# Kernel tuning notes

Hardware: AMD Instinct MI355X
Metric: run time of the kernel (lower is better)

The kernel has to match this reference:

```python
import jax, jax.numpy as jnp
import numpy as np
import math

B = 2
D_MODEL = 2048
L_MAX = 4096
FILTER_ORDER = 64
EMB_DIM = 3
SHORT_K = 3


def setup_inputs() -> dict:
    key = jax.random.key(0)
    ks = jax.random.split(key, 16)
    D = D_MODEL

    def n(k, shape, scale=0.02):
        return jax.random.normal(k, shape, dtype=jnp.float32) * scale

    return {
        "x": jax.random.normal(ks[0], (B, L_MAX, D), dtype=jnp.float32),
        "in_proj_w": n(ks[1], (3 * D, D)),
        "in_proj_b": n(ks[2], (3 * D,)),
        "short_w": n(ks[3], (3 * D, 1, SHORT_K), 0.3),   # depthwise conv weight (O, I/groups=1, K)
        "short_b": n(ks[4], (3 * D,), 0.1),
        "mlp_w0": n(ks[5], (FILTER_ORDER, EMB_DIM), 0.5),
        "mlp_b0": n(ks[6], (FILTER_ORDER,), 0.5),
        "sin_freq": jnp.ones((1, FILTER_ORDER), dtype=jnp.float32),  # Sin module, w=1, shared across MLP layers
        "mlp_w1": n(ks[7], (FILTER_ORDER, FILTER_ORDER), 0.1),
        "mlp_b1": n(ks[8], (FILTER_ORDER,), 0.1),
        "mlp_w2": n(ks[9], (FILTER_ORDER, FILTER_ORDER), 0.1),
        "mlp_b2": n(ks[10], (FILTER_ORDER,), 0.1),
        "mlp_w3": n(ks[11], (D, FILTER_ORDER), 0.1),      # final Linear(order -> d_model, bias=False)
        "filter_bias": jax.random.normal(ks[12], (D,), dtype=jnp.float32),  # HyenaFilter.bias ~ randn
        "out_proj_w": n(ks[13], (D, D)),
        "out_proj_b": n(ks[14], (D,)),
    }


def _pos_emb(L):
    # PositionalEmbedding: t in [0,1], 1 complex band (emb_dim=3 -> bands=1)
    t = jnp.linspace(0.0, 1.0, L)[:, None]               # (L, 1)
    t_resc = jnp.linspace(0.0, L - 1.0, L)
    w = 2.0 * math.pi * t_resc / L                       # (L,)
    bands = (EMB_DIM - 1) // 2
    f = jnp.linspace(1e-4, bands - 1.0, bands)           # (bands,)
    ang = f[None, :] * w[:, None]                        # (L, bands)
    # z = exp(-1j * f * w) -> real = cos, imag = -sin
    z = jnp.concatenate([t, jnp.cos(ang), -jnp.sin(ang)], axis=-1)  # (L, 3)
    return z, t


def _filter_k(L, w0, b0, freq, w1, b1, w2, b2, w3):
    z, t = _pos_emb(L)
    h = jnp.sin(freq * (z @ w0.T + b0))
    h = jnp.sin(freq * (h @ w1.T + b1))
    h = jnp.sin(freq * (h @ w2.T + b2))
    h = h @ w3.T                                         # (L, D)
    # ExponentialModulation: deltas = linspace(log(.01)/1.5, log(.01)/0.3, D)
    max_decay = math.log(0.01) / 0.3
    min_decay = math.log(0.01) / 1.5
    deltas = jnp.linspace(min_decay, max_decay, h.shape[-1])
    decay = jnp.exp(-t * jnp.abs(deltas)[None, :])       # (L, D)
    return (h * decay).T                                 # (D, L)


def _fftconv(u, k, bias):
    # fftconv_ref with gelu=False, no dropout_mask: u (B, D, L), k (D, L), bias (D,)
    L = u.shape[-1]
    n = 2 * L
    k_f = jnp.fft.rfft(k, n=n) / n                       # (D, L+1)
    u_f = jnp.fft.rfft(u, n=n)                           # (B, D, L+1)
    y = jnp.fft.irfft(u_f * k_f, n=n, norm="forward")[..., :L]
    return y + u * bias[:, None]


def reference(x, in_proj_w, in_proj_b, short_w, short_b, mlp_w0, mlp_b0, sin_freq,
              mlp_w1, mlp_b1, mlp_w2, mlp_b2, mlp_w3, filter_bias,
              out_proj_w, out_proj_b):
    Bn, L, D = x.shape
    u = x @ in_proj_w.T + in_proj_b                      # (B, L, 3D)
    u = jnp.transpose(u, (0, 2, 1))                      # (B, 3D, L)
    # depthwise short conv, padding = short_k - 1, truncate to L (causal-ish)
    uc = jax.lax.conv_general_dilated(
        u, short_w, window_strides=(1,),
        padding=[(SHORT_K - 1, SHORT_K - 1)],
        feature_group_count=3 * D,
        dimension_numbers=("NCH", "OIH", "NCH"))
    uc = uc[..., :L] + short_b[None, :, None]
    x0, x1, v = jnp.split(uc, 3, axis=1)                 # each (B, D, L)
    k = _filter_k(L, mlp_w0, mlp_b0, sin_freq, mlp_w1, mlp_b1, mlp_w2, mlp_b2, mlp_w3)
    # order=2 Hyena recurrence: single gated long-conv step
    v = v * x1
    v = _fftconv(v, k, filter_bias)
    y = v * x0                                           # (B, D, L)
    y = jnp.transpose(y, (0, 2, 1))                      # (B, L, D)
    return y @ out_proj_w.T + out_proj_b
```

## Files before the change

### kernel.cpp

```cpp
#include <hip/hip_runtime.h>
#include <hip/hip_bf16.h>
#include <cstdint>
#include <cstddef>

typedef __attribute__((ext_vector_type(8))) short    bf16x8;
typedef __attribute__((ext_vector_type(4))) float    f32x4;
typedef __attribute__((ext_vector_type(8))) unsigned short u16x8;
typedef __attribute__((ext_vector_type(4))) float    f32v4;
typedef __attribute__((ext_vector_type(4))) unsigned short u16v4;

__device__ __forceinline__ float b2f(unsigned short v) {
    return __builtin_bit_cast(float, ((unsigned int)v) << 16);
}
__device__ __forceinline__ unsigned short f2b(float f) {
    unsigned int u = __builtin_bit_cast(unsigned int, f);
    u += 0x7fffu + ((u >> 16) & 1u);
    return (unsigned short)(u >> 16);
}

__device__ __forceinline__ void async16(const void* g, void* l) {
    __builtin_amdgcn_global_load_lds(
        (const __attribute__((address_space(1))) unsigned int*)g,
        (__attribute__((address_space(3))) unsigned int*)l, 16, 0, 0);
}

__global__ __launch_bounds__(256) void cvt_f32_bf16(const float* __restrict__ src,
                                                    unsigned short* __restrict__ dst, int n4) {
    int i = blockIdx.x * blockDim.x + threadIdx.x;
    int stride = gridDim.x * blockDim.x;
    const f32v4* s4 = (const f32v4*)src;
    u16v4* d4 = (u16v4*)dst;
    for (; i < n4; i += stride) {
        f32v4 v = s4[i];
        u16v4 o;
        o.x = f2b(v.x); o.y = f2b(v.y); o.z = f2b(v.z); o.w = f2b(v.w);
        d4[i] = o;
    }
}

template <int MODE>
__global__ __launch_bounds__(256, 2) void gemm_bf16(
    const unsigned short* __restrict__ A,
    const unsigned short* __restrict__ Bw,
    const float* __restrict__ bias,
    void* __restrict__ Cout,
    int M, int N, int K, int Lseq, int CH)
{
    constexpr int SMEM_N = (MODE == 1) ? 16384 : 8192;
    __shared__ unsigned short smem[SMEM_N];

    const int tid  = threadIdx.x;
    const int w    = tid >> 6;
    const int lane = tid & 63;
    const int quad = lane >> 4;
    const int lq   = lane & 15;
    const int n0 = blockIdx.x * 128;
    const int m0 = blockIdx.y * 128;
    const int wave_m = w & 1, wave_n = w >> 1;

    const int rSub = w * 32 + (lane >> 2);
    const int kcol = (lane & 3) * 8;
    const unsigned short* pA0 = A  + (size_t)(m0 + rSub)      * K + kcol;
    const unsigned short* pA1 = A  + (size_t)(m0 + rSub + 16) * K + kcol;
    const unsigned short* pB0 = Bw + (size_t)(n0 + rSub)      * K + kcol;
    const unsigned short* pB1 = Bw + (size_t)(n0 + rSub + 16) * K + kcol;
    char* sb = (char*)smem;
    char* dA0 = sb + w * 2048;
    char* dA1 = sb + w * 2048 + 1024;
    char* dB0 = sb + 8192 + w * 2048;
    char* dB1 = sb + 8192 + w * 2048 + 1024;

    f32x4 acc[4][4] = {};

    const int nIter = K >> 5;
    for (int kt = 0; kt < nIter; ++kt) {
        async16(pA0, dA0); async16(pA1, dA1);
        async16(pB0, dB0); async16(pB1, dB1);
        pA0 += 32; pA1 += 32; pB0 += 32; pB1 += 32;
        __syncthreads();
        bf16x8 af[4], bw[4];
        #pragma unroll
        for (int i = 0; i < 4; ++i) {
            af[i] = *(const bf16x8*)&smem[(wave_m * 64 + i * 16 + lq) * 32 + quad * 8];
            bw[i] = *(const bf16x8*)&smem[4096 + (wave_n * 64 + i * 16 + lq) * 32 + quad * 8];
        }
        #pragma unroll
        for (int i = 0; i < 4; ++i)
            #pragma unroll
            for (int j = 0; j < 4; ++j)
                acc[i][j] = __builtin_amdgcn_mfma_f32_16x16x32_bf16(af[i], bw[j], acc[i][j], 0, 0, 0);
        __syncthreads();
    }

    if (MODE == 0) {
        float* out = (float*)Cout;
        #pragma unroll
        for (int j = 0; j < 4; ++j) {
            const int col = n0 + wave_n * 64 + j * 16 + lq;
            const float bv = bias[col];
            #pragma unroll
            for (int i = 0; i < 4; ++i) {
                const int rowb = m0 + wave_m * 64 + i * 16 + quad * 4;
                f32x4 c = acc[i][j];
                out[(size_t)(rowb + 0) * N + col] = c.x + bv;
                out[(size_t)(rowb + 1) * N + col] = c.y + bv;
                out[(size_t)(rowb + 2) * N + col] = c.z + bv;
                out[(size_t)(rowb + 3) * N + col] = c.w + bv;
            }
        }
    } else {
        #pragma unroll
        for (int j = 0; j < 4; ++j) {
            const int nl = wave_n * 64 + j * 16 + lq;
            const float bv = bias[n0 + nl];
            #pragma unroll
            for (int i = 0; i < 4; ++i) {
                const int ml = wave_m * 64 + i * 16 + quad * 4;
                f32x4 c = acc[i][j];
                smem[nl * 128 + ml + 0] = f2b(c.x + bv);
                smem[nl * 128 + ml + 1] = f2b(c.y + bv);
                smem[nl * 128 + ml + 2] = f2b(c.z + bv);
                smem[nl * 128 + ml + 3] = f2b(c.w + bv);
            }
        }
        __syncthreads();
        unsigned short* uo = (unsigned short*)Cout;
        const int bI = m0 >> 12;
        const int l0 = m0 & 4095;
        for (int e = tid; e < 2048; e += 256) {
            const int nl = e >> 4, seg = e & 15;
            u16x8 v = *(const u16x8*)&smem[nl * 128 + seg * 8];
            *(u16x8*)&uo[(size_t)(bI * CH + n0 + nl) * Lseq + l0 + seg * 8] = v;
        }
    }
}

__global__ __launch_bounds__(256) void filter_kernel(
    const float* __restrict__ w0, const float* __restrict__ b0,
    const float* __restrict__ freq,
    const float* __restrict__ w1, const float* __restrict__ b1,
    const float* __restrict__ w2, const float* __restrict__ b2,
    const float* __restrict__ w3, float* __restrict__ kf)
{
    __shared__ float ha[64][64];
    __shared__ float hb[64][64];
    const int tid = threadIdx.x;
    const int l0 = blockIdx.x * 64;
    const int d0 = blockIdx.y * 256;
    const int l  = tid & 63;
    const int lg = l0 + l;
    const float tt = (float)lg * (1.0f / 4095.0f);
    const float wang = 6.283185307179586f * (float)lg * (1.0f / 4096.0f);
    const float a  = 1e-4f * wang;
    const float z0 = tt, z1 = cosf(a), z2 = -sinf(a);

    for (int e = tid; e < 4096; e += 256) {
        const int dim = e >> 6;
        float pre = z0 * w0[dim * 3] + z1 * w0[dim * 3 + 1] + z2 * w0[dim * 3 + 2] + b0[dim];
        ha[dim][l] = sinf(freq[dim] * pre);
    }
    __syncthreads();
    for (int e = tid; e < 4096; e += 256) {
        const int dim = e >> 6;
        float acc = b1[dim];
        #pragma unroll
        for (int jj = 0; jj < 64; ++jj) acc += w1[dim * 64 + jj] * ha[jj][l];
        hb[dim][l] = sinf(freq[dim] * acc);
    }
    __syncthreads();
    for (int e = tid; e < 4096; e += 256) {
        const int dim = e >> 6;
        float acc = b2[dim];
        #pragma unroll
        for (int jj = 0; jj < 64; ++jj) acc += w2[dim * 64 + jj] * hb[jj][l];
        ha[dim][l] = sinf(freq[dim] * acc);
    }
    __syncthreads();
    for (int d = d0 + (tid >> 6); d < d0 + 256; d += 4) {
        float acc = 0.f;
        #pragma unroll
        for (int jj = 0; jj < 64; ++jj) acc += w3[d * 64 + jj] * ha[jj][l];
        const float delta = fabsf(-3.0701134573253944f + (-5.999245642062483e-3f) * (float)d);
        kf[(size_t)d * 4096 + lg] = acc * __expf(-tt * delta);
    }
}

#define PIDX(i) ((i) + ((i) >> 5))

__device__ __forceinline__ void bfly_f(float& r1, float& i1, float& r2, float& i2, float wr, float wi) {
    float ur = r1, ui = i1, vr = r2, vi = i2;
    r1 = ur + vr; i1 = ui + vi;
    float dr = ur - vr, di = ui - vi;
    r2 = dr * wr - di * wi;
    i2 = dr * wi + di * wr;
}
__device__ __forceinline__ void bfly_i(float& r1, float& i1, float& r2, float& i2, float wr, float wi) {
    float vr = r2 * wr - i2 * wi, vi = r2 * wi + i2 * wr;
    float ur = r1, ui = i1;
    r1 = ur + vr; i1 = ui + vi;
    r2 = ur - vr; i2 = ui - vi;
}

template <int DS, int STR>
__device__ __forceinline__ void fwd_stage(float* re, float* im, int tt) {
    float wr[8], wi[8];
    constexpr float c = -3.14159265358979f / (float)(STR * DS);
    #pragma unroll
    for (int k = 0; k < DS; ++k) __sincosf(c * (float)(tt + STR * k), &wi[k], &wr[k]);
    #pragma unroll
    for (int s = 0; s < 16; ++s)
        if ((s & DS) == 0)
            bfly_f(re[s], im[s], re[s + DS], im[s + DS], wr[s & (DS - 1)], wi[s & (DS - 1)]);
}
template <int DS, int STR>
__device__ __forceinline__ void inv_stage(float* re, float* im, int tt) {
    float wr[8], wi[8];
    constexpr float c = 3.14159265358979f / (float)(STR * DS);
    #pragma unroll
    for (int k = 0; k < DS; ++k) __sincosf(c * (float)(tt + STR * k), &wi[k], &wr[k]);
    #pragma unroll
    for (int s = 0; s < 16; ++s)
        if ((s & DS) == 0)
            bfly_i(re[s], im[s], re[s + DS], im[s + DS], wr[s & (DS - 1)], wi[s & (DS - 1)]);
}

__device__ __forceinline__ void xchg(float* re, float* im, float* fre, float* fim,
                                     int wbase, int wstr, int rbase, int rstr) {
    __syncthreads();
    #pragma unroll
    for (int s = 0; s < 16; ++s) {
        const int i = wbase + wstr * s;
        fre[PIDX(i)] = re[s]; fim[PIDX(i)] = im[s];
    }
    __syncthreads();
    #pragma unroll
    for (int s = 0; s < 16; ++s) {
        const int i = rbase + rstr * s;
        re[s] = fre[PIDX(i)]; im[s] = fim[PIDX(i)];
    }
}

__device__ __forceinline__ void fwd_fft(float* re, float* im, float* fre, float* fim, int t) {
    const int off = t & 31, seg = t >> 5;
    fwd_stage<8, 512>(re, im, t);
    fwd_stage<4, 512>(re, im, t);
    fwd_stage<2, 512>(re, im, t);
    fwd_stage<1, 512>(re, im, t);
    xchg(re, im, fre, fim, t, 512, seg * 512 + off, 32);
    fwd_stage<8, 32>(re, im, off);
    fwd_stage<4, 32>(re, im, off);
    fwd_stage<2, 32>(re, im, off);
    fwd_stage<1, 32>(re, im, off);
    {
        float wr, wi;
        __sincosf(-3.14159265358979f * (float)(off & 15) / 16.0f, &wi, &wr);
        const bool hi = (off & 16) != 0;
        #pragma unroll
        for (int s = 0; s < 16; ++s) {
            float rr = __shfl_xor(re[s], 16);
            float ri = __shfl_xor(im[s], 16);
            if (!hi) { re[s] += rr; im[s] += ri; }
            else {
                float dr = rr - re[s], di = ri - im[s];
                re[s] = dr * wr - di * wi;
                im[s] = dr * wi + di * wr;
            }
        }
    }
    xchg(re, im, fre, fim, seg * 512 + off, 32, 16 * t, 1);
    fwd_stage<8, 1>(re, im, 0);
    fwd_stage<4, 1>(re, im, 0);
    fwd_stage<2, 1>(re, im, 0);
    fwd_stage<1, 1>(re, im, 0);
}

__device__ __forceinline__ void inv_fft(float* re, float* im, float* fre, float* fim, int t) {
    const int off = t & 31, seg = t >> 5;
    inv_stage<1, 1>(re, im, 0);
    inv_stage<2, 1>(re, im, 0);
    inv_stage<4, 1>(re, im, 0);
    inv_stage<8, 1>(re, im, 0);
    xchg(re, im, fre, fim, 16 * t, 1, seg * 512 + off, 32);
    {
        float wr, wi;
        __sincosf(3.14159265358979f * (float)(off & 15) / 16.0f, &wi, &wr);
        const bool hi = (off & 16) != 0;
        #pragma unroll
        for (int s = 0; s < 16; ++s) {
            float rr = __shfl_xor(re[s], 16);
            float ri = __shfl_xor(im[s], 16);
            if (!hi) {
                float vr = rr * wr - ri * wi, vi = rr * wi + ri * wr;
                re[s] += vr; im[s] += vi;
            } else {
                float vr = re[s] * wr - im[s] * wi, vi = re[s] * wi + im[s] * wr;
                re[s] = rr - vr; im[s] = ri - vi;
            }
        }
    }
    inv_stage<1, 32>(re, im, off);
    inv_stage<2, 32>(re, im, off);
    inv_stage<4, 32>(re, im, off);
    inv_stage<8, 32>(re, im, off);
    xchg(re, im, fre, fim, seg * 512 + off, 32, t, 512);
    inv_stage<1, 512>(re, im, t);
    inv_stage<2, 512>(re, im, t);
    inv_stage<4, 512>(re, im, t);
    inv_stage<8, 512>(re, im, t);
}

__global__ __launch_bounds__(512, 2) void kfft_kernel(
    const float* __restrict__ kf,
    float* __restrict__ kspec)
{
    __shared__ float fre[8448];
    __shared__ float fim[8448];
    const int t = threadIdx.x;
    const int d = blockIdx.x;
    float kr[16], ki[16];
    #pragma unroll
    for (int s = 0; s < 16; ++s) {
        kr[s] = (s < 8) ? kf[(size_t)d * 4096 + t + 512 * s] : 0.f;
        ki[s] = 0.f;
    }
    fwd_fft(kr, ki, fre, fim, t);
    f32x4* kv = (f32x4*)kspec + (size_t)d * 4096 + t;
    #pragma unroll
    for (int q = 0; q < 8; ++q) {
        f32x4 o;
        o.x = kr[2 * q]; o.y = ki[2 * q];
        o.z = kr[2 * q + 1]; o.w = ki[2 * q + 1];
        kv[q * 512] = o;
    }
}

__global__ __launch_bounds__(512, 2) void hyena_fft_kernel(
    const unsigned short* __restrict__ u,
    const float* __restrict__ kspec,
    const float* __restrict__ sw,
    const float* __restrict__ sbv,
    const float* __restrict__ fbias,
    unsigned short* __restrict__ zb)
{
    __shared__ float fre[8448];
    __shared__ float fim[8448];
    const int t = threadIdx.x;
    const int d = blockIdx.x;

    const int c0 = d, c1 = 2048 + d, c2 = 4096 + d;
    const float w00 = sw[c0*3+0], w01 = sw[c0*3+1], w02 = sw[c0*3+2], bb0 = sbv[c0];
    const float w10 = sw[c1*3+0], w11 = sw[c1*3+1], w12 = sw[c1*3+2], bb1 = sbv[c1];
    const float w20 = sw[c2*3+0], w21 = sw[c2*3+1], w22 = sw[c2*3+2], bb2 = sbv[c2];
    const float fb = fbias[d];

    float vgr_[2][8], x0r_[2][8];
    float xr[16], xi[16];
    #pragma unroll
    for (int s = 0; s < 8; ++s) {
        const int l = t + (s << 9);
        #pragma unroll
        for (int b = 0; b < 2; ++b) {
            const size_t base = (size_t)b * 6144 * 4096;
            const size_t r0 = base + (size_t)c0 * 4096;
            const size_t r1 = base + (size_t)c1 * 4096;
            const size_t r2 = base + (size_t)c2 * 4096;
            const float a0 = b2f(u[r0 + l]);
            const float a1 = (l >= 1) ? b2f(u[r0 + l - 1]) : 0.f;
            const float a2 = (l >= 2) ? b2f(u[r0 + l - 2]) : 0.f;
            const float x0v = w00 * a2 + w01 * a1 + w02 * a0 + bb0;
            const float e0 = b2f(u[r1 + l]);
            const float e1 = (l >= 1) ? b2f(u[r1 + l - 1]) : 0.f;
            const float e2 = (l >= 2) ? b2f(u[r1 + l - 2]) : 0.f;
            const float x1v = w10 * e2 + w11 * e1 + w12 * e0 + bb1;
            const float g0 = b2f(u[r2 + l]);
            const float g1 = (l >= 1) ? b2f(u[r2 + l - 1]) : 0.f;
            const float g2 = (l >= 2) ? b2f(u[r2 + l - 2]) : 0.f;
            const float vv = w20 * g2 + w21 * g1 + w22 * g0 + bb2;
            const float vg = vv * x1v;
            vgr_[b][s] = vg; x0r_[b][s] = x0v;
            if (b == 0) xr[s] = vg; else xi[s] = vg;
        }
    }
    #pragma unroll
    for (int s = 8; s < 16; ++s) { xr[s] = 0.f; xi[s] = 0.f; }

    fwd_fft(xr, xi, fre, fim, t);
    {
        const f32x4* kv = (const f32x4*)kspec + (size_t)d * 4096 + t;
        f32x4 kk[8];
        #pragma unroll
        for (int q = 0; q < 8; ++q) kk[q] = kv[q * 512];
        #pragma unroll
        for (int q = 0; q < 8; ++q) {
            float cr = xr[2 * q], ci = xi[2 * q];
            xr[2 * q] = cr * kk[q].x - ci * kk[q].y;
            xi[2 * q] = cr * kk[q].y + ci * kk[q].x;
            cr = xr[2 * q + 1]; ci = xi[2 * q + 1];
            xr[2 * q + 1] = cr * kk[q].z - ci * kk[q].w;
            xi[2 * q + 1] = cr * kk[q].w + ci * kk[q].z;
        }
    }
    inv_fft(xr, xi, fre, fim, t);

    const float inv_n = 1.0f / 8192.0f;
    #pragma unroll
    for (int s = 0; s < 8; ++s) {
        const int p = t + (s << 9);
        const float z0 = (xr[s] * inv_n + vgr_[0][s] * fb) * x0r_[0][s];
        const float z1 = (xi[s] * inv_n + vgr_[1][s] * fb) * x0r_[1][s];
        zb[(size_t)d * 4096 + p]          = f2b(z0);
        zb[(size_t)(2048 + d) * 4096 + p] = f2b(z1);
    }
}

__global__ __launch_bounds__(256) void transpose_kernel(const unsigned short* __restrict__ zb,
                                                        unsigned short* __restrict__ zt)
{
    __shared__ unsigned int tile[64][65];
    const int l0 = blockIdx.x * 64, d0 = blockIdx.y * 64, b = blockIdx.z;
    const int tid = threadIdx.x;
    for (int e = tid; e < 4096; e += 256) {
        const int r = e >> 6, c = e & 63;
        tile[r][c] = zb[(size_t)(b * 2048 + d0 + r) * 4096 + l0 + c];
    }
    __syncthreads();
    for (int e = tid; e < 4096; e += 256) {
        const int r = e >> 6, c = e & 63;
        zt[(size_t)(b * 4096 + l0 + r) * 2048 + d0 + c] = (unsigned short)tile[c][r];
    }
}

extern "C" void kernel_launch(void* const* d_in, const int* in_sizes, int n_in,
                              void* d_out, int out_size, void* d_ws, size_t ws_size,
                              hipStream_t stream)
{
    const float* x   = (const float*)d_in[0];
    const float* ipw = (const float*)d_in[1];
    const float* ipb = (const float*)d_in[2];
    const float* sw  = (const float*)d_in[3];
    const float* sb  = (const float*)d_in[4];
    const float* w0  = (const float*)d_in[5];
    const float* b0  = (const float*)d_in[6];
    const float* fr  = (const float*)d_in[7];
    const float* w1  = (const float*)d_in[8];
    const float* b1  = (const float*)d_in[9];
    const float* w2  = (const float*)d_in[10];
    const float* b2  = (const float*)d_in[11];
    const float* w3  = (const float*)d_in[12];
    const float* fb  = (const float*)d_in[13];
    const float* opw = (const float*)d_in[14];
    const float* opb = (const float*)d_in[15];
    float* out = (float*)d_out;

    char* ws = (char*)d_ws;
    unsigned short* xb    = (unsigned short*)ws;
    unsigned short* wbi   = (unsigned short*)(ws + 33554432);
    float*          kspec = (float*)ws;
    unsigned short* ztb   = (unsigned short*)ws;
    unsigned short* wbo   = (unsigned short*)(ws + 33554432);
    unsigned short* ub    = (unsigned short*)(ws + 134217728);
    float*          kf    = (float*)(ws + 234881024);
    unsigned short* zbm   = (unsigned short*)(ws + 234881024);

    cvt_f32_bf16<<<1024, 256, 0, stream>>>(x,   xb,  16777216 / 4);
    cvt_f32_bf16<<<1024, 256, 0, stream>>>(ipw, wbi, 12582912 / 4);

    gemm_bf16<1><<<dim3(48, 64), 256, 0, stream>>>(xb, wbi, ipb, ub, 8192, 6144, 2048, 4096, 6144);

    filter_kernel<<<dim3(64, 8), 256, 0, stream>>>(w0, b0, fr, w1, b1, w2, b2, w3, kf);

    kfft_kernel<<<2048, 512, 0, stream>>>(kf, kspec);

    hyena_fft_kernel<<<2048, 512, 0, stream>>>(ub, kspec, sw, sb, fb, zbm);

    transpose_kernel<<<dim3(64, 32, 2), 256, 0, stream>>>(zbm, ztb);

    cvt_f32_bf16<<<512,  256, 0, stream>>>(opw, wbo, 4194304 / 4);

    gemm_bf16<0><<<dim3(16, 64), 256, 0, stream>>>(ztb, wbo, opb, out, 8192, 2048, 2048, 4096, 2048);
}
```

Measured before the change: 836.2 us.

## Replace GEMM with 256x256 tile, double-buffered, swizzled LDS pipelined kernel

Replaces the 128x128, single-stage bf16 GEMM with a 512-thread 256x256-tile kernel. It uses a K-step of 64 with double-buffered LDS staging via async global-to-LDS loads, an XOR-swizzled LDS layout, and phased MFMA issue with setprio and barriers. The block index is remapped across XCDs, and the epilogue uses padded LDS with vectorized stores. The goal is to cut global memory traffic, improve data reuse per block and overlap loads with MFMA work. In exchange it uses far more LDS per block (about 128KB) and allows only one block per CU, which also leaves fewer blocks (256) for the output projection.

```diff
diff --git a/kernel.cpp b/kernel.cpp
--- a/kernel.cpp
+++ b/kernel.cpp
@@ -39,69 +39,134 @@
 }
 
 template <int MODE>
-__global__ __launch_bounds__(256, 2) void gemm_bf16(
+__global__ __launch_bounds__(512, 1) void gemm256(
     const unsigned short* __restrict__ A,
     const unsigned short* __restrict__ Bw,
     const float* __restrict__ bias,
     void* __restrict__ Cout,
-    int M, int N, int K, int Lseq, int CH)
+    int M, int N, int K, int Lseq, int CH, int ntn)
 {
-    constexpr int SMEM_N = (MODE == 1) ? 16384 : 8192;
-    __shared__ unsigned short smem[SMEM_N];
-
-    const int tid  = threadIdx.x;
-    const int w    = tid >> 6;
-    const int lane = tid & 63;
-    const int quad = lane >> 4;
-    const int lq   = lane & 15;
-    const int n0 = blockIdx.x * 128;
-    const int m0 = blockIdx.y * 128;
-    const int wave_m = w & 1, wave_n = w >> 1;
-
-    const int rSub = w * 32 + (lane >> 2);
-    const int kcol = (lane & 3) * 8;
-    const unsigned short* pA0 = A  + (size_t)(m0 + rSub)      * K + kcol;
-    const unsigned short* pA1 = A  + (size_t)(m0 + rSub + 16) * K + kcol;
-    const unsigned short* pB0 = Bw + (size_t)(n0 + rSub)      * K + kcol;
-    const unsigned short* pB1 = Bw + (size_t)(n0 + rSub + 16) * K + kcol;
-    char* sb = (char*)smem;
-    char* dA0 = sb + w * 2048;
-    char* dA1 = sb + w * 2048 + 1024;
-    char* dB0 = sb + 8192 + w * 2048;
-    char* dB1 = sb + 8192 + w * 2048 + 1024;
-
-    f32x4 acc[4][4] = {};
-
-    const int nIter = K >> 5;
-    for (int kt = 0; kt < nIter; ++kt) {
-        async16(pA0, dA0); async16(pA1, dA1);
-        async16(pB0, dB0); async16(pB1, dB1);
-        pA0 += 32; pA1 += 32; pB0 += 32; pB1 += 32;
-        __syncthreads();
-        bf16x8 af[4], bw[4];
-        #pragma unroll
-        for (int i = 0; i < 4; ++i) {
-            af[i] = *(const bf16x8*)&smem[(wave_m * 64 + i * 16 + lq) * 32 + quad * 8];
-            bw[i] = *(const bf16x8*)&smem[4096 + (wave_n * 64 + i * 16 + lq) * 32 + quad * 8];
-        }
-        #pragma unroll
-        for (int i = 0; i < 4; ++i)
-            #pragma unroll
-            for (int j = 0; j < 4; ++j)
-                acc[i][j] = __builtin_amdgcn_mfma_f32_16x16x32_bf16(af[i], bw[j], acc[i][j], 0, 0, 0);
-        __syncthreads();
+    constexpr int SMEM_BYTES = (MODE == 1) ? 135168 : 131072;
+    __shared__ char smemc[SMEM_BYTES];
+
+    const int tid = threadIdx.x;
+    const int w   = tid >> 6;
+    const int l   = tid & 63;
+    const int wm  = w & 1;
+    const int wn  = w >> 1;
+    const int quad = l >> 4;
+    const int lq   = l & 15;
+
+    int id = blockIdx.x;
+    const int q8 = gridDim.x >> 3;
+    id = (id & 7) * q8 + (id >> 3);
+    const int bx = id % ntn, by = id / ntn;
+    const int n0 = bx * 256, m0 = by * 256;
+
+    const int su0 = quad ^ (lq & 7);
+    const int su1 = su0 ^ 4;
+
+    uint32_t offAe[2][2], offBe[2][2];
+    int dA[2][2], dB[2][2];
+    #pragma unroll
+    for (int h = 0; h < 2; ++h)
+        #pragma unroll
+        for (int c = 0; c < 2; ++c) {
+            const int Lr = h * 128 + w * 16 + c * 8 + (l >> 3);
+            const int gA = ((Lr & 64) << 1) | ((Lr & 128) >> 1) | (Lr & 63);
+            const int u  = (l & 7) ^ (l >> 3);
+            offAe[h][c] = (uint32_t)(m0 + gA) * (uint32_t)K + (uint32_t)(u * 8);
+            offBe[h][c] = (uint32_t)(n0 + Lr) * (uint32_t)K + (uint32_t)(u * 8);
+            const int rb = (h * 128 + w * 16 + c * 8) * 128;
+            dA[h][c] = rb;
+            dB[h][c] = 32768 + rb;
+        }
+
+#define STAGE_A(bs, h, tile) do { \
+    async16(A + offAe[h][0] + (size_t)(tile) * 64, smemc + ((bs) * 65536 + dA[h][0])); \
+    async16(A + offAe[h][1] + (size_t)(tile) * 64, smemc + ((bs) * 65536 + dA[h][1])); \
+} while (0)
+#define STAGE_B(bs, h, tile) do { \
+    async16(Bw + offBe[h][0] + (size_t)(tile) * 64, smemc + ((bs) * 65536 + dB[h][0])); \
+    async16(Bw + offBe[h][1] + (size_t)(tile) * 64, smemc + ((bs) * 65536 + dB[h][1])); \
+} while (0)
+
+    f32x4 acc[8][4] = {};
+    bf16x8 bw[4][2], a[2][2];
+
+#define LDB8(bs) do { \
+    _Pragma("unroll") for (int j = 0; j < 4; ++j) { \
+        const int Lr = wn * 64 + j * 16 + lq; \
+        bw[j][0] = *(const bf16x8*)(smemc + (bs) * 65536 + 32768 + Lr * 128 + su0 * 16); \
+        bw[j][1] = *(const bf16x8*)(smemc + (bs) * 65536 + 32768 + Lr * 128 + su1 * 16); \
+    } } while (0)
+#define LDA4(bs, q) do { \
+    _Pragma("unroll") for (int mf = 0; mf < 2; ++mf) { \
+        const int g = wm * 128 + (q) * 32 + mf * 16 + lq; \
+        const int Lr = ((g & 64) << 1) | ((g & 128) >> 1) | (g & 63); \
+        a[mf][0] = *(const bf16x8*)(smemc + (bs) * 65536 + Lr * 128 + su0 * 16); \
+        a[mf][1] = *(const bf16x8*)(smemc + (bs) * 65536 + Lr * 128 + su1 * 16); \
+    } } while (0)
+#define MFMA16(q) do { \
+    _Pragma("unroll") for (int mf = 0; mf < 2; ++mf) \
+    _Pragma("unroll") for (int j = 0; j < 4; ++j) \
+    _Pragma("unroll") for (int kk = 0; kk < 2; ++kk) \
+        acc[(q) * 2 + mf][j] = __builtin_amdgcn_mfma_f32_16x16x32_bf16(a[mf][kk], bw[j][kk], acc[(q) * 2 + mf][j], 0, 0, 0); \
+} while (0)
+#define PHASE_SYNC() do { \
+    __builtin_amdgcn_s_barrier(); \
+    asm volatile("s_waitcnt lgkmcnt(0)" ::: "memory"); \
+    __builtin_amdgcn_sched_barrier(0); \
+    __builtin_amdgcn_s_setprio(1); \
+} while (0)
+#define PHASE_END() do { \
+    __builtin_amdgcn_s_setprio(0); \
+    __builtin_amdgcn_s_barrier(); \
+} while (0)
+#define PHASE_END_DRAIN(lastf) do { \
+    __builtin_amdgcn_s_setprio(0); \
+    if (lastf) asm volatile("s_waitcnt vmcnt(0)" ::: "memory"); \
+    else       asm volatile("s_waitcnt vmcnt(6)" ::: "memory"); \
+    __builtin_amdgcn_s_barrier(); \
+} while (0)
+
+    STAGE_B(0, 0, 0); STAGE_B(0, 1, 0); STAGE_A(0, 0, 0); STAGE_A(0, 1, 0);
+    STAGE_B(1, 0, 1); STAGE_B(1, 1, 1); STAGE_A(1, 0, 1);
+    asm volatile("s_waitcnt vmcnt(6)" ::: "memory");
+    __builtin_amdgcn_s_barrier();
+
+    const int nIt = K >> 7;
+    for (int i = 0; i < nIt; ++i) {
+        const bool last = (i == nIt - 1);
+        const int t0 = 2 * i, t1 = 2 * i + 1;
+        LDB8(0); LDA4(0, 0); STAGE_A(1, 1, t1);
+        PHASE_SYNC(); MFMA16(0); PHASE_END();
+        LDA4(0, 1); if (!last) STAGE_B(0, 0, t0 + 2);
+        PHASE_SYNC(); MFMA16(1); PHASE_END();
+        LDA4(0, 2); if (!last) STAGE_B(0, 1, t0 + 2);
+        PHASE_SYNC(); MFMA16(2); PHASE_END();
+        LDA4(0, 3); if (!last) STAGE_A(0, 0, t0 + 2);
+        PHASE_SYNC(); MFMA16(3); PHASE_END_DRAIN(last);
+        LDB8(1); LDA4(1, 0); if (!last) STAGE_A(0, 1, t0 + 2);
+        PHASE_SYNC(); MFMA16(0); PHASE_END();
+        LDA4(1, 1); if (!last) STAGE_B(1, 0, t1 + 2);
+        PHASE_SYNC(); MFMA16(1); PHASE_END();
+        LDA4(1, 2); if (!last) STAGE_B(1, 1, t1 + 2);
+        PHASE_SYNC(); MFMA16(2); PHASE_END();
+        LDA4(1, 3); if (!last) STAGE_A(1, 0, t1 + 2);
+        PHASE_SYNC(); MFMA16(3); PHASE_END_DRAIN(last);
     }
 
     if (MODE == 0) {
         float* out = (float*)Cout;
         #pragma unroll
         for (int j = 0; j < 4; ++j) {
-            const int col = n0 + wave_n * 64 + j * 16 + lq;
+            const int col = n0 + wn * 64 + j * 16 + lq;
             const float bv = bias[col];
             #pragma unroll
-            for (int i = 0; i < 4; ++i) {
-                const int rowb = m0 + wave_m * 64 + i * 16 + quad * 4;
-                f32x4 c = acc[i][j];
+            for (int i8 = 0; i8 < 8; ++i8) {
+                const int rowb = m0 + wm * 128 + i8 * 16 + quad * 4;
+                f32x4 c = acc[i8][j];
                 out[(size_t)(rowb + 0) * N + col] = c.x + bv;
                 out[(size_t)(rowb + 1) * N + col] = c.y + bv;
                 out[(size_t)(rowb + 2) * N + col] = c.z + bv;
@@ -109,30 +174,40 @@
             }
         }
     } else {
+        unsigned short* sE = (unsigned short*)smemc;
+        __syncthreads();
         #pragma unroll
         for (int j = 0; j < 4; ++j) {
-            const int nl = wave_n * 64 + j * 16 + lq;
+            const int nl = wn * 64 + j * 16 + lq;
             const float bv = bias[n0 + nl];
             #pragma unroll
-            for (int i = 0; i < 4; ++i) {
-                const int ml = wave_m * 64 + i * 16 + quad * 4;
-                f32x4 c = acc[i][j];
-                smem[nl * 128 + ml + 0] = f2b(c.x + bv);
-                smem[nl * 128 + ml + 1] = f2b(c.y + bv);
-                smem[nl * 128 + ml + 2] = f2b(c.z + bv);
-                smem[nl * 128 + ml + 3] = f2b(c.w + bv);
+            for (int i8 = 0; i8 < 8; ++i8) {
+                const int ml = wm * 128 + i8 * 16 + quad * 4;
+                f32x4 c = acc[i8][j];
+                u16v4 pk;
+                pk.x = f2b(c.x + bv); pk.y = f2b(c.y + bv);
+                pk.z = f2b(c.z + bv); pk.w = f2b(c.w + bv);
+                *(u16v4*)&sE[nl * 264 + ml] = pk;
             }
         }
         __syncthreads();
         unsigned short* uo = (unsigned short*)Cout;
         const int bI = m0 >> 12;
         const int l0 = m0 & 4095;
-        for (int e = tid; e < 2048; e += 256) {
-            const int nl = e >> 4, seg = e & 15;
-            u16x8 v = *(const u16x8*)&smem[nl * 128 + seg * 8];
+        for (int e = tid; e < 8192; e += 512) {
+            const int nl = e >> 5, seg = e & 31;
+            u16x8 v = *(const u16x8*)&sE[nl * 264 + seg * 8];
             *(u16x8*)&uo[(size_t)(bI * CH + n0 + nl) * Lseq + l0 + seg * 8] = v;
         }
     }
+#undef STAGE_A
+#undef STAGE_B
+#undef LDB8
+#undef LDA4
+#undef MFMA16
+#undef PHASE_SYNC
+#undef PHASE_END
+#undef PHASE_END_DRAIN
 }
 
 __global__ __launch_bounds__(256) void filter_kernel(
@@ -465,7 +540,7 @@
     cvt_f32_bf16<<<1024, 256, 0, stream>>>(x,   xb,  16777216 / 4);
     cvt_f32_bf16<<<1024, 256, 0, stream>>>(ipw, wbi, 12582912 / 4);
 
-    gemm_bf16<1><<<dim3(48, 64), 256, 0, stream>>>(xb, wbi, ipb, ub, 8192, 6144, 2048, 4096, 6144);
+    gemm256<1><<<768, 512, 0, stream>>>(xb, wbi, ipb, ub, 8192, 6144, 2048, 4096, 6144, 24);
 
     filter_kernel<<<dim3(64, 8), 256, 0, stream>>>(w0, b0, fr, w1, b1, w2, b2, w3, kf);
 
@@ -477,5 +552,5 @@
 
     cvt_f32_bf16<<<512,  256, 0, stream>>>(opw, wbo, 4194304 / 4);
 
-    gemm_bf16<0><<<dim3(16, 64), 256, 0, stream>>>(ztb, wbo, opb, out, 8192, 2048, 2048, 4096, 2048);
-}
+    gemm256<0><<<256, 512, 0, stream>>>(ztb, wbo, opb, out, 8192, 2048, 2048, 4096, 2048, 8);
+}
```

New measurement: 765.9 us. 8.4% less time.
